# Performance work log

Measured on AMD Instinct MI355X. Metric: run time of the kernel, lower is better.

Reference implementation:

```python
import jax, jax.numpy as jnp
import numpy as np
from jax import lax

WIN = 7          # win_size
K1 = 0.01
K2 = 0.03
NP_W = WIN * WIN
COV_NORM = NP_W / (NP_W - 1)


def _box_filter(x):
    w = jnp.ones((1, 1, WIN, WIN), x.dtype) / NP_W
    return lax.conv_general_dilated(
        x, w, window_strides=(1, 1), padding='VALID',
        dimension_numbers=('NCHW', 'OIHW', 'NCHW'))


def setup_inputs() -> dict:
    key = jax.random.key(0)
    k1, k2 = jax.random.split(key)
    B, C, T, H, W = 16, 1, 20, 256, 256
    Xt = jax.random.uniform(k1, (B, C, T, H, W), dtype=jnp.float32)
    Yt = jax.random.uniform(k2, (B, C, T, H, W), dtype=jnp.float32)
    data_range = jnp.ones((1,), dtype=jnp.float32)  # unused: overwritten per frame
    return {"Xt": Xt, "Yt": Yt, "data_range": data_range}


def reference(Xt, Yt, data_range):
    B, C, T, H, W = Xt.shape
    # Fold time into batch: frame index = b*T + t
    X = Xt.transpose(0, 2, 1, 3, 4).reshape(B * T, C, H, W)
    Y = Yt.transpose(0, 2, 1, 3, 4).reshape(B * T, C, H, W)

    # Per-frame data_range = max over the whole batch slice Yt[:,:,t]
    # (torch.Tensor([Y.max()]) detaches it from autograd in the original)
    dr = lax.stop_gradient(jnp.max(Yt, axis=(0, 1, 3, 4)))      # [T]
    dr = jnp.tile(dr, B)[:, None, None, None]                   # [B*T,1,1,1]
    C1 = (K1 * dr) ** 2
    C2 = (K2 * dr) ** 2

    # One conv call over 5 stacked moment maps
    stacked = jnp.concatenate([X, Y, X * X, Y * Y, X * Y], axis=0)
    filt = _box_filter(stacked)
    ux, uy, uxx, uyy, uxy = jnp.split(filt, 5, axis=0)

    vx = COV_NORM * (uxx - ux * ux)
    vy = COV_NORM * (uyy - uy * uy)
    vxy = COV_NORM * (uxy - ux * uy)

    A1 = 2 * ux * uy + C1
    A2 = 2 * vxy + C2
    B1 = ux * ux + uy * uy + C1
    B2 = vx + vy + C2
    S = (A1 * A2) / (B1 * B2)

    # sum_t (1 - mean(S_t)) / T == 1 - mean(S) since every frame has equal count
    return 1.0 - jnp.mean(S)
```

## Files before the change

### kernel.cpp

```cpp
#include <hip/hip_runtime.h>


#define HH 256
#define WW 256
#define OUTW 250
#define NT 20
#define NB 16
#define NFRAMES (NT * NB)
#define STRIPS 10
#define RPS 25
#define NBLK2 (NFRAMES * STRIPS)

__device__ __forceinline__ float wave_sum(float v) {
#pragma unroll
    for (int off = 32; off > 0; off >>= 1) v += __shfl_down(v, off, 64);
    return v;
}
__device__ __forceinline__ float wave_max(float v) {
#pragma unroll
    for (int off = 32; off > 0; off >>= 1) v = fmaxf(v, __shfl_down(v, off, 64));
    return v;
}

__global__ __launch_bounds__(256) void dr_max_kernel(const float* __restrict__ Y,
                                                     unsigned* __restrict__ dr_bits) {
    int t = blockIdx.x;
    int bq = blockIdx.y;
    const float4* p = (const float4*)(Y + (size_t)((bq >> 2) * NT + t) * (HH * WW))
                      + (bq & 3) * 4096;
    float m = 0.f;
#pragma unroll 4
    for (int k = 0; k < 16; ++k) {
        float4 v = p[k * 256 + threadIdx.x];
        m = fmaxf(m, fmaxf(fmaxf(v.x, v.y), fmaxf(v.z, v.w)));
    }
    m = wave_max(m);
    __shared__ float smax[4];
    int lane = threadIdx.x & 63, w = threadIdx.x >> 6;
    if (lane == 0) smax[w] = m;
    __syncthreads();
    if (threadIdx.x == 0) {
        float mm = fmaxf(fmaxf(smax[0], smax[1]), fmaxf(smax[2], smax[3]));
        atomicMax(dr_bits + t, __float_as_uint(mm));
    }
}

__device__ __forceinline__ float ssim_px(float hx, float hy, float hxx, float hyy,
                                         float hxy, float C1, float C2) {
    const float inv_np = 1.0f / 49.0f;
    const float cov = 49.0f / 48.0f;
    float ux = hx * inv_np, uy = hy * inv_np;
    float uxx = hxx * inv_np, uyy = hyy * inv_np, uxy = hxy * inv_np;
    float vx = cov * (uxx - ux * ux);
    float vy = cov * (uyy - uy * uy);
    float vxy = cov * (uxy - ux * uy);
    float A1 = 2.f * ux * uy + C1, A2 = 2.f * vxy + C2;
    float B1 = ux * ux + uy * uy + C1, B2 = vx + vy + C2;
    return (A1 * A2) * __builtin_amdgcn_rcpf(B1 * B2);
}

__device__ __forceinline__ float4 taps7(float4 s, const float* halo ) {
    float4 ha = *(const float4*)halo;
    float2 hb = *(const float2*)(halo + 4);
    float o0 = s.x + s.y + s.z + s.w + ha.x + ha.y + ha.z;
    float o1 = o0 - s.x + ha.w;
    float o2 = o1 - s.y + hb.x;
    float o3 = o2 - s.z + hb.y;
    return make_float4(o0, o1, o2, o3);
}

#define LSW (WW + 16)

__global__ __launch_bounds__(64) void ssim_kernel(const float* __restrict__ X,
                                                  const float* __restrict__ Y,
                                                  const float* __restrict__ dr_arr,
                                                  float* __restrict__ partials) {
    __shared__ __align__(16) float ls[5][LSW];
    int bid = blockIdx.x;
    int frame = bid / STRIPS;
    int strip = bid % STRIPS;
    int t = frame % NT;
    const float4* x4 = (const float4*)(X + (size_t)frame * (HH * WW));
    const float4* y4 = (const float4*)(Y + (size_t)frame * (HH * WW));
    int l = threadIdx.x;
    int c0 = 4 * l;

    float dr = dr_arr[t];
    float C1 = (0.01f * dr) * (0.01f * dr);
    float C2 = (0.03f * dr) * (0.03f * dr);

    int r0 = strip * RPS;

    float4 sx = make_float4(0, 0, 0, 0), sy = sx, sxx = sx, syy = sx, sxy = sx;
#pragma unroll
    for (int dy = 0; dy < 7; ++dy) {
        float4 xv = x4[(r0 + dy) * 64 + l];
        float4 yv = y4[(r0 + dy) * 64 + l];
        sx.x += xv.x; sx.y += xv.y; sx.z += xv.z; sx.w += xv.w;
        sy.x += yv.x; sy.y += yv.y; sy.z += yv.z; sy.w += yv.w;
        sxx.x += xv.x * xv.x; sxx.y += xv.y * xv.y; sxx.z += xv.z * xv.z; sxx.w += xv.w * xv.w;
        syy.x += yv.x * yv.x; syy.y += yv.y * yv.y; syy.z += yv.z * yv.z; syy.w += yv.w * yv.w;
        sxy.x += xv.x * yv.x; sxy.y += xv.y * yv.y; sxy.z += xv.z * yv.z; sxy.w += xv.w * yv.w;
    }

    float acc = 0.f;
    for (int r = r0; r < r0 + RPS; ++r) {
        *(float4*)&ls[0][c0] = sx;
        *(float4*)&ls[1][c0] = sy;
        *(float4*)&ls[2][c0] = sxx;
        *(float4*)&ls[3][c0] = syy;
        *(float4*)&ls[4][c0] = sxy;

        bool more = (r + 1 < r0 + RPS);
        float4 xo, yo, xn, yn;
        if (more) {
            xo = x4[r * 64 + l];       yo = y4[r * 64 + l];
            xn = x4[(r + 7) * 64 + l]; yn = y4[(r + 7) * 64 + l];
        }
        __syncthreads();

        float4 hx  = taps7(sx,  &ls[0][c0 + 4]);
        float4 hy  = taps7(sy,  &ls[1][c0 + 4]);
        float4 hxx = taps7(sxx, &ls[2][c0 + 4]);
        float4 hyy = taps7(syy, &ls[3][c0 + 4]);
        float4 hxy = taps7(sxy, &ls[4][c0 + 4]);
        __syncthreads();

        if (c0 + 0 < OUTW) acc += ssim_px(hx.x, hy.x, hxx.x, hyy.x, hxy.x, C1, C2);
        if (c0 + 1 < OUTW) acc += ssim_px(hx.y, hy.y, hxx.y, hyy.y, hxy.y, C1, C2);
        if (c0 + 2 < OUTW) acc += ssim_px(hx.z, hy.z, hxx.z, hyy.z, hxy.z, C1, C2);
        if (c0 + 3 < OUTW) acc += ssim_px(hx.w, hy.w, hxx.w, hyy.w, hxy.w, C1, C2);

        if (more) {
            sx.x += xn.x - xo.x; sx.y += xn.y - xo.y; sx.z += xn.z - xo.z; sx.w += xn.w - xo.w;
            sy.x += yn.x - yo.x; sy.y += yn.y - yo.y; sy.z += yn.z - yo.z; sy.w += yn.w - yo.w;
            sxx.x += xn.x * xn.x - xo.x * xo.x; sxx.y += xn.y * xn.y - xo.y * xo.y;
            sxx.z += xn.z * xn.z - xo.z * xo.z; sxx.w += xn.w * xn.w - xo.w * xo.w;
            syy.x += yn.x * yn.x - yo.x * yo.x; syy.y += yn.y * yn.y - yo.y * yo.y;
            syy.z += yn.z * yn.z - yo.z * yo.z; syy.w += yn.w * yn.w - yo.w * yo.w;
            sxy.x += xn.x * yn.x - xo.x * yo.x; sxy.y += xn.y * yn.y - xo.y * yo.y;
            sxy.z += xn.z * yn.z - xo.z * yo.z; sxy.w += xn.w * yn.w - xo.w * yo.w;
        }
    }

    acc = wave_sum(acc);
    if (l == 0) partials[bid] = acc;
}

__global__ __launch_bounds__(256) void final_kernel(const float* __restrict__ partials,
                                                    float* __restrict__ out) {
    float s = 0.f;
    for (int i = threadIdx.x; i < NBLK2; i += 256) s += partials[i];
    s = wave_sum(s);
    __shared__ float ssum[4];
    int lane = threadIdx.x & 63, w = threadIdx.x >> 6;
    if (lane == 0) ssum[w] = s;
    __syncthreads();
    if (threadIdx.x == 0) {
        float total = ssum[0] + ssum[1] + ssum[2] + ssum[3];
        const double denom = (double)NFRAMES * OUTW * OUTW;
        out[0] = (float)(1.0 - (double)total / denom);
    }
}

extern "C" void kernel_launch(void* const* d_in, const int* in_sizes, int n_in,
                              void* d_out, int out_size, void* d_ws, size_t ws_size,
                              hipStream_t stream) {
    const float* X = (const float*)d_in[0];
    const float* Y = (const float*)d_in[1];

    float* ws = (float*)d_ws;
    unsigned* dr_bits = (unsigned*)ws;
    float* partials   = ws + 32;

    hipMemsetAsync(d_ws, 0, NT * sizeof(float), stream);

    dim3 g1(NT, NB * 4);
    hipLaunchKernelGGL(dr_max_kernel, g1, dim3(256), 0, stream, Y, dr_bits);
    hipLaunchKernelGGL(ssim_kernel, dim3(NBLK2), dim3(64), 0, stream,
                       X, Y, (const float*)ws, partials);
    hipLaunchKernelGGL(final_kernel, dim3(1), dim3(256), 0, stream,
                       partials, (float*)d_out);
}
```

Baseline: 217.1 us.

## Pack four independent strip waves per block and replace barriers with compiler fences

Each 256-thread block now runs four independent waves, each handling its own frame strip with a private LDS slice. Because a wave only reads LDS it wrote itself, the __syncthreads barriers become compiler-only memory fences, which removes block-level barrier stalls. The per-pixel SSIM math is rescaled to work on raw window sums, with constants premultiplied by 2401, so the 1/49 multiplies drop out and FMAs can be used. This relies on wave-synchronous LDS ordering and slightly changes floating-point rounding.

Result: no change. 218.3 us (+0.5%).

```diff
diff --git a/kernel.cpp b/kernel.cpp
--- a/kernel.cpp
+++ b/kernel.cpp
@@ -9,7 +9,11 @@
 #define NFRAMES (NT * NB)
 #define STRIPS 10
 #define RPS 25
-#define NBLK2 (NFRAMES * STRIPS)
+#define NWAVES (NFRAMES * STRIPS)
+#define WPB 4
+#define NBLK2 (NWAVES / WPB)
+
+#define LDS_FENCE() asm volatile("" ::: "memory")
 
 __device__ __forceinline__ float wave_sum(float v) {
 #pragma unroll
@@ -45,17 +49,18 @@
     }
 }
 
+
 __device__ __forceinline__ float ssim_px(float hx, float hy, float hxx, float hyy,
-                                         float hxy, float C1, float C2) {
-    const float inv_np = 1.0f / 49.0f;
+                                         float hxy, float c1, float c2) {
     const float cov = 49.0f / 48.0f;
-    float ux = hx * inv_np, uy = hy * inv_np;
-    float uxx = hxx * inv_np, uyy = hyy * inv_np, uxy = hxy * inv_np;
-    float vx = cov * (uxx - ux * ux);
-    float vy = cov * (uyy - uy * uy);
-    float vxy = cov * (uxy - ux * uy);
-    float A1 = 2.f * ux * uy + C1, A2 = 2.f * vxy + C2;
-    float B1 = ux * ux + uy * uy + C1, B2 = vx + vy + C2;
+    float hx2 = hx * hx, hy2 = hy * hy, hxy1 = hx * hy;
+    float A1 = __builtin_fmaf(2.f, hxy1, c1);
+    float B1 = hx2 + hy2 + c1;
+    float t1 = __builtin_fmaf(49.f, hxx, -hx2);
+    float t2 = __builtin_fmaf(49.f, hyy, -hy2);
+    float t3 = __builtin_fmaf(49.f, hxy, -hxy1);
+    float A2 = __builtin_fmaf(2.f * cov, t3, c2);
+    float B2 = __builtin_fmaf(cov, t1 + t2, c2);
     return (A1 * A2) * __builtin_amdgcn_rcpf(B1 * B2);
 }
 
@@ -71,23 +76,25 @@
 
 #define LSW (WW + 16)
 
-__global__ __launch_bounds__(64) void ssim_kernel(const float* __restrict__ X,
-                                                  const float* __restrict__ Y,
-                                                  const float* __restrict__ dr_arr,
-                                                  float* __restrict__ partials) {
-    __shared__ __align__(16) float ls[5][LSW];
-    int bid = blockIdx.x;
-    int frame = bid / STRIPS;
-    int strip = bid % STRIPS;
+__global__ __launch_bounds__(256) void ssim_kernel(const float* __restrict__ X,
+                                                   const float* __restrict__ Y,
+                                                   const float* __restrict__ dr_arr,
+                                                   float* __restrict__ partials) {
+    __shared__ __align__(16) float ls_all[WPB][5][LSW];
+    int w = threadIdx.x >> 6;
+    int l = threadIdx.x & 63;
+    int wid = blockIdx.x * WPB + w;
+    int frame = wid / STRIPS;
+    int strip = wid % STRIPS;
     int t = frame % NT;
     const float4* x4 = (const float4*)(X + (size_t)frame * (HH * WW));
     const float4* y4 = (const float4*)(Y + (size_t)frame * (HH * WW));
-    int l = threadIdx.x;
+    float (*ls)[LSW] = ls_all[w];
     int c0 = 4 * l;
 
     float dr = dr_arr[t];
-    float C1 = (0.01f * dr) * (0.01f * dr);
-    float C2 = (0.03f * dr) * (0.03f * dr);
+    float c1 = 2401.f * (0.01f * dr) * (0.01f * dr);
+    float c2 = 2401.f * (0.03f * dr) * (0.03f * dr);
 
     int r0 = strip * RPS;
 
@@ -117,19 +124,21 @@
             xo = x4[r * 64 + l];       yo = y4[r * 64 + l];
             xn = x4[(r + 7) * 64 + l]; yn = y4[(r + 7) * 64 + l];
         }
-        __syncthreads();
+
+        LDS_FENCE();
 
         float4 hx  = taps7(sx,  &ls[0][c0 + 4]);
         float4 hy  = taps7(sy,  &ls[1][c0 + 4]);
         float4 hxx = taps7(sxx, &ls[2][c0 + 4]);
         float4 hyy = taps7(syy, &ls[3][c0 + 4]);
         float4 hxy = taps7(sxy, &ls[4][c0 + 4]);
-        __syncthreads();
 
-        if (c0 + 0 < OUTW) acc += ssim_px(hx.x, hy.x, hxx.x, hyy.x, hxy.x, C1, C2);
-        if (c0 + 1 < OUTW) acc += ssim_px(hx.y, hy.y, hxx.y, hyy.y, hxy.y, C1, C2);
-        if (c0 + 2 < OUTW) acc += ssim_px(hx.z, hy.z, hxx.z, hyy.z, hxy.z, C1, C2);
-        if (c0 + 3 < OUTW) acc += ssim_px(hx.w, hy.w, hxx.w, hyy.w, hxy.w, C1, C2);
+        LDS_FENCE();
+
+        if (c0 + 0 < OUTW) acc += ssim_px(hx.x, hy.x, hxx.x, hyy.x, hxy.x, c1, c2);
+        if (c0 + 1 < OUTW) acc += ssim_px(hx.y, hy.y, hxx.y, hyy.y, hxy.y, c1, c2);
+        if (c0 + 2 < OUTW) acc += ssim_px(hx.z, hy.z, hxx.z, hyy.z, hxy.z, c1, c2);
+        if (c0 + 3 < OUTW) acc += ssim_px(hx.w, hy.w, hxx.w, hyy.w, hxy.w, c1, c2);
 
         if (more) {
             sx.x += xn.x - xo.x; sx.y += xn.y - xo.y; sx.z += xn.z - xo.z; sx.w += xn.w - xo.w;
@@ -144,13 +153,13 @@
     }
 
     acc = wave_sum(acc);
-    if (l == 0) partials[bid] = acc;
+    if (l == 0) partials[wid] = acc;
 }
 
 __global__ __launch_bounds__(256) void final_kernel(const float* __restrict__ partials,
                                                     float* __restrict__ out) {
     float s = 0.f;
-    for (int i = threadIdx.x; i < NBLK2; i += 256) s += partials[i];
+    for (int i = threadIdx.x; i < NWAVES; i += 256) s += partials[i];
     s = wave_sum(s);
     __shared__ float ssum[4];
     int lane = threadIdx.x & 63, w = threadIdx.x >> 6;
@@ -177,7 +186,7 @@
 
     dim3 g1(NT, NB * 4);
     hipLaunchKernelGGL(dr_max_kernel, g1, dim3(256), 0, stream, Y, dr_bits);
-    hipLaunchKernelGGL(ssim_kernel, dim3(NBLK2), dim3(64), 0, stream,
+    hipLaunchKernelGGL(ssim_kernel, dim3(NBLK2), dim3(256), 0, stream,
                        X, Y, (const float*)ws, partials);
     hipLaunchKernelGGL(final_kernel, dim3(1), dim3(256), 0, stream,
                        partials, (float*)d_out);
```
